# Kernel optimization log

Measured on AMD Instinct MI355X. Metric: run time of the kernel, lower is better.

Reference implementation:

```python
import jax, jax.numpy as jnp
import numpy as np

D_MODEL = 2048
NUM_HEADS = 32
NUM_GROUPS = 8
HEAD_DIM = D_MODEL // NUM_HEADS  # 64
HPG = NUM_HEADS // NUM_GROUPS    # heads per group = 4
B, S = 2, 2048


def setup_inputs() -> dict:
    key = jax.random.key(0)
    ks = jax.random.split(key, 11)
    sd = 1.0 / np.sqrt(D_MODEL)
    kv_dim = HEAD_DIM * NUM_GROUPS
    return {
        "q": jax.random.normal(ks[0], (B, S, D_MODEL), jnp.float32),
        "k": jax.random.normal(ks[1], (B, S, D_MODEL), jnp.float32),
        "v": jax.random.normal(ks[2], (B, S, D_MODEL), jnp.float32),
        "Wq": jax.random.normal(ks[3], (D_MODEL, D_MODEL), jnp.float32) * sd,
        "bq": jnp.zeros((D_MODEL,), jnp.float32),
        "Wk": jax.random.normal(ks[4], (D_MODEL, kv_dim), jnp.float32) * sd,
        "bk": jnp.zeros((kv_dim,), jnp.float32),
        "Wv": jax.random.normal(ks[5], (D_MODEL, kv_dim), jnp.float32) * sd,
        "bv": jnp.zeros((kv_dim,), jnp.float32),
        "Wo": jax.random.normal(ks[6], (D_MODEL, D_MODEL), jnp.float32) * sd,
        "bo": jnp.zeros((D_MODEL,), jnp.float32),
    }


def reference(q, k, v, Wq, bq, Wk, bk, Wv, bv, Wo, bo):
    b, qlen, _ = q.shape
    kvlen = k.shape[1]
    # projections
    qh = (q @ Wq + bq).reshape(b, qlen, NUM_GROUPS, HPG, HEAD_DIM)   # [b,s,g,h,d]
    kh = (k @ Wk + bk).reshape(b, kvlen, NUM_GROUPS, HEAD_DIM)        # [b,t,g,d]
    vh = (v @ Wv + bv).reshape(b, kvlen, NUM_GROUPS, HEAD_DIM)        # [b,t,g,d]
    scale = 1.0 / np.sqrt(HEAD_DIM).astype(np.float32)
    # grouped attention: each group's heads share the same K/V
    scores = jnp.einsum('bsghd,btgd->bghst', qh, kh) * scale          # [b,g,h,s,t]
    attn = jax.nn.softmax(scores, axis=-1)                            # dropout = identity (eval)
    out = jnp.einsum('bghst,btgd->bsghd', attn, vh)                   # [b,s,g,h,d]
    out = out.reshape(b, qlen, D_MODEL)
    return out @ Wo + bo
```

## Files before the change

### kernel.cpp

```cpp
#include <hip/hip_runtime.h>

typedef unsigned short u16;
typedef unsigned int u32;
typedef __attribute__((ext_vector_type(8))) short bf16x8;
typedef __attribute__((ext_vector_type(4))) float f32x4;
typedef __attribute__((ext_vector_type(16))) float f32x16;

#define DM 2048
#define SQ_SCALE (0.125f * 1.44269504089f)

__device__ __forceinline__ u16 f2bf(float f) {
  union { float f; u32 u; } v; v.f = f;
  u32 r = v.u + 0x7fffu + ((v.u >> 16) & 1u);
  return (u16)(r >> 16);
}
__device__ __forceinline__ u32 pkrn(float lo, float hi) {
  union { float f; u32 u; } a, b; a.f = lo; b.f = hi;
  return ((a.u + 0x8000u) >> 16) | ((b.u + 0x8000u) & 0xffff0000u);
}
__device__ __forceinline__ u32 cvtpk(float lo, float hi) {
  u32 r;
  asm("v_cvt_pk_bf16_f32 %0, %1, %2" : "=v"(r) : "v"(lo), "v"(hi));
  return r;
}
__device__ __forceinline__ void gload16(const u16* g, u16* l) {
  __builtin_amdgcn_global_load_lds((const __attribute__((address_space(1))) void*)g,
                                   (__attribute__((address_space(3))) void*)l, 16, 0, 0);
}

__global__ __launch_bounds__(256) void cast3(const float* __restrict__ a0,
                                             const float* __restrict__ a1,
                                             const float* __restrict__ a2,
                                             u16* __restrict__ o0,
                                             u16* __restrict__ o1,
                                             u16* __restrict__ o2) {
  const float* in; u16* out;
  if (blockIdx.z == 0) { in = a0; out = o0; }
  else if (blockIdx.z == 1) { in = a1; out = o1; }
  else { in = a2; out = o2; }
  size_t i = ((size_t)blockIdx.x * 256 + threadIdx.x) * 8;
  float4 f0 = *(const float4*)(in + i);
  float4 f1 = *(const float4*)(in + i + 4);
  uint4 w = {pkrn(f0.x, f0.y), pkrn(f0.z, f0.w), pkrn(f1.x, f1.y), pkrn(f1.z, f1.w)};
  *(uint4*)(out + i) = w;
}

__global__ __launch_bounds__(256) void transpose_cast(const float* __restrict__ in,
                                                      u16* __restrict__ out,
                                                      int K, int N) {
  __shared__ u16 s[64][72];
  int n0 = blockIdx.x * 64, k0 = blockIdx.y * 64;
  int t = threadIdx.x;
  int r = t >> 2;
  int cc = (t & 3) * 16;
  const float* ip = in + (size_t)(k0 + r) * N + n0 + cc;
  u16 tmp[16];
#pragma unroll
  for (int i = 0; i < 16; i += 4) {
    float4 v = *(const float4*)(ip + i);
    tmp[i] = f2bf(v.x); tmp[i + 1] = f2bf(v.y);
    tmp[i + 2] = f2bf(v.z); tmp[i + 3] = f2bf(v.w);
  }
  *(uint4*)&s[r][cc] = *(uint4*)tmp;
  *(uint4*)&s[r][cc + 8] = *(uint4*)(tmp + 8);
  __syncthreads();
#pragma unroll
  for (int i = 0; i < 16; i++) tmp[i] = s[cc + i][r];
  u16* op = out + (size_t)(n0 + r) * K + k0 + cc;
  *(uint4*)op = *(uint4*)tmp;
  *(uint4*)(op + 8) = *(uint4*)(tmp + 8);
}

__global__ __launch_bounds__(256) void gemm_proj(const u16* __restrict__ qb,
                                                 const u16* __restrict__ kb,
                                                 const u16* __restrict__ vb,
                                                 const u16* __restrict__ Bt,
                                                 const float* __restrict__ bqp,
                                                 const float* __restrict__ bkp,
                                                 const float* __restrict__ bvp,
                                                 u16* __restrict__ qhb,
                                                 u16* __restrict__ kvb,
                                                 u16* __restrict__ vtb) {
  __shared__ u16 As[128 * 32];
  __shared__ u16 Bs[128 * 32];
  int n0 = blockIdx.x * 128, m0 = blockIdx.y * 128;
  const u16* A; const float* bias; u16* C; int cw, bofs; float esc;
  if (n0 < 2048)      { A = qb; bias = bqp; C = qhb; cw = 2048; bofs = 0;    esc = SQ_SCALE; }
  else if (n0 < 2560) { A = kb; bias = bkp; C = kvb; cw = 1024; bofs = 2048; esc = 1.0f; }
  else                { A = vb; bias = bvp; C = kvb; cw = 1024; bofs = 2560; esc = 1.0f; }
  int ccol0 = (n0 < 2048) ? n0 : (n0 - 2048);

  int tid = threadIdx.x, wave = tid >> 6, lane = tid & 63;
  int lq = lane & 15, quad = lane >> 4;
  int wm = (wave & 1) * 64, wn = (wave >> 1) * 64;

  f32x4 zero = {0.f, 0.f, 0.f, 0.f};
  f32x4 acc[4][4];
#pragma unroll
  for (int i = 0; i < 4; i++)
#pragma unroll
    for (int j = 0; j < 4; j++) acc[i][j] = zero;

  const u16* gA = A + (size_t)(m0 + wave * 16 + (lane >> 2)) * 2048 + (lane & 3) * 8;
  const u16* gB = Bt + (size_t)(n0 + wave * 16 + (lane >> 2)) * 2048 + (lane & 3) * 8;
  u16* lA0 = &As[(wave * 16) * 32];
  u16* lA1 = &As[(64 + wave * 16) * 32];
  u16* lB0 = &Bs[(wave * 16) * 32];
  u16* lB1 = &Bs[(64 + wave * 16) * 32];

  for (int k0 = 0; k0 < 2048; k0 += 32) {
    __syncthreads();
    gload16(gA + k0, lA0);
    gload16(gA + (size_t)64 * 2048 + k0, lA1);
    gload16(gB + k0, lB0);
    gload16(gB + (size_t)64 * 2048 + k0, lB1);
    __syncthreads();
    bf16x8 af[4], bf[4];
#pragma unroll
    for (int i = 0; i < 4; i++) af[i] = *(const bf16x8*)&As[(wm + i * 16 + lq) * 32 + quad * 8];
#pragma unroll
    for (int j = 0; j < 4; j++) bf[j] = *(const bf16x8*)&Bs[(wn + j * 16 + lq) * 32 + quad * 8];
#pragma unroll
    for (int i = 0; i < 4; i++)
#pragma unroll
      for (int j = 0; j < 4; j++)
        acc[i][j] = __builtin_amdgcn_mfma_f32_16x16x32_bf16(af[i], bf[j], acc[i][j], 0, 0, 0);
  }
  if (n0 >= 2560) {
#pragma unroll
    for (int j = 0; j < 4; j++) {
      int cv = (n0 - 2560) + wn + j * 16 + lq;
      float bvv = bias[cv];
      u16* vout = vtb + (size_t)cv * 2048;
#pragma unroll
      for (int i = 0; i < 4; i++) {
        int row = m0 + wm + i * 16 + quad * 4;
        int bb = row >> 11, tt = row & 2047;
        u16 w4[4];
#pragma unroll
        for (int rg = 0; rg < 4; rg++) w4[rg] = f2bf(acc[i][j][rg] + bvv);
        *(uint2*)(vout + (size_t)bb * 8 * 64 * 2048 + tt) = *(uint2*)w4;
      }
    }
  } else {
#pragma unroll
    for (int j = 0; j < 4; j++) {
      int nglob = n0 + wn + j * 16 + lq;
      float bv = bias[nglob - bofs];
      int col = ccol0 + wn + j * 16 + lq;
#pragma unroll
      for (int i = 0; i < 4; i++) {
#pragma unroll
        for (int rg = 0; rg < 4; rg++) {
          int row = m0 + wm + i * 16 + quad * 4 + rg;
          C[(size_t)row * cw + col] = f2bf((acc[i][j][rg] + bv) * esc);
        }
      }
    }
  }
}

__global__ __launch_bounds__(256) void gemm_o(const u16* __restrict__ A,
                                              const u16* __restrict__ Bt,
                                              const float* __restrict__ bias,
                                              float* __restrict__ C) {
  __shared__ u16 As[128 * 32];
  __shared__ u16 Bs[128 * 32];
  int n0 = blockIdx.x * 128, m0 = blockIdx.y * 128;
  int tid = threadIdx.x, wave = tid >> 6, lane = tid & 63;
  int lq = lane & 15, quad = lane >> 4;
  int wm = (wave & 1) * 64, wn = (wave >> 1) * 64;

  f32x4 zero = {0.f, 0.f, 0.f, 0.f};
  f32x4 acc[4][4];
#pragma unroll
  for (int i = 0; i < 4; i++)
#pragma unroll
    for (int j = 0; j < 4; j++) acc[i][j] = zero;

  const u16* gA = A + (size_t)(m0 + wave * 16 + (lane >> 2)) * 2048 + (lane & 3) * 8;
  const u16* gB = Bt + (size_t)(n0 + wave * 16 + (lane >> 2)) * 2048 + (lane & 3) * 8;
  u16* lA0 = &As[(wave * 16) * 32];
  u16* lA1 = &As[(64 + wave * 16) * 32];
  u16* lB0 = &Bs[(wave * 16) * 32];
  u16* lB1 = &Bs[(64 + wave * 16) * 32];

  for (int k0 = 0; k0 < 2048; k0 += 32) {
    __syncthreads();
    gload16(gA + k0, lA0);
    gload16(gA + (size_t)64 * 2048 + k0, lA1);
    gload16(gB + k0, lB0);
    gload16(gB + (size_t)64 * 2048 + k0, lB1);
    __syncthreads();
    bf16x8 af[4], bf[4];
#pragma unroll
    for (int i = 0; i < 4; i++) af[i] = *(const bf16x8*)&As[(wm + i * 16 + lq) * 32 + quad * 8];
#pragma unroll
    for (int j = 0; j < 4; j++) bf[j] = *(const bf16x8*)&Bs[(wn + j * 16 + lq) * 32 + quad * 8];
#pragma unroll
    for (int i = 0; i < 4; i++)
#pragma unroll
      for (int j = 0; j < 4; j++)
        acc[i][j] = __builtin_amdgcn_mfma_f32_16x16x32_bf16(af[i], bf[j], acc[i][j], 0, 0, 0);
  }
#pragma unroll
  for (int j = 0; j < 4; j++) {
    int col = n0 + wn + j * 16 + lq;
    float bv = bias[col];
#pragma unroll
    for (int i = 0; i < 4; i++) {
#pragma unroll
      for (int rg = 0; rg < 4; rg++) {
        int row = m0 + wm + i * 16 + quad * 4 + rg;
        C[(size_t)row * 2048 + col] = acc[i][j][rg] + bv;
      }
    }
  }
}

__global__ __launch_bounds__(256) void attn2(const u16* __restrict__ qh,
                                             const u16* __restrict__ kvb,
                                             const u16* __restrict__ vtb,
                                             u16* __restrict__ out) {
  __shared__ u16 Ks[2][32][72];
  __shared__ u16 Vs[2][64][40];
  __shared__ float Ls[4][32];
  int flat = blockIdx.x + (blockIdx.y << 4);
  int w = ((flat & 7) << 7) + (flat >> 3);
  int head = w >> 4;
  int b = head >> 5, g = (head >> 2) & 7, h = head & 3;
  int tid = threadIdx.x, wave = tid >> 6, lane = tid & 63;
  int lh = lane & 31, hi = lane >> 5;
  const int qoff = (g * 4 + h) * 64;
  const int koff = g * 64;
  int sBase = (w & 15) * 128 + wave * 32;

  bf16x8 qf[4];
#pragma unroll
  for (int st = 0; st < 4; st++)
    qf[st] = *(const bf16x8*)(qh + (size_t)(b * 2048 + sBase + lh) * DM +
                              qoff + st * 16 + hi * 8);

  f32x16 o_acc[2];
#pragma unroll
  for (int db = 0; db < 2; db++)
#pragma unroll
    for (int r = 0; r < 16; r++) o_acc[db][r] = 0.f;
  float l_acc = 0.f;

  int sr = tid >> 3, sc = (tid & 7) * 8;
  int vd = tid >> 2, vc = (tid & 3) * 8;
  const u16* kbase = kvb + (size_t)b * 2048 * 1024 + koff;
  const u16* vbase = vtb + (size_t)(head >> 2) * 64 * 2048 + (size_t)vd * 2048;

  uint4 kreg = *(const uint4*)(kbase + (size_t)sr * 1024 + sc);
  uint4 vreg = *(const uint4*)(vbase + vc);

  int c = 0;
  for (int t0 = 0; t0 < 2048; t0 += 32) {
    *(uint4*)&Ks[c][sr][sc] = kreg;
    *(uint4*)&Vs[c][vd][vc] = vreg;
    int tn = (t0 + 32 < 2048) ? t0 + 32 : 0;
    kreg = *(const uint4*)(kbase + (size_t)(tn + sr) * 1024 + sc);
    vreg = *(const uint4*)(vbase + tn + vc);
    __syncthreads();

    bf16x8 kf[4], vf[2][2];
#pragma unroll
    for (int st = 0; st < 4; st++) kf[st] = *(const bf16x8*)&Ks[c][lh][st * 16 + hi * 8];
#pragma unroll
    for (int T = 0; T < 2; T++)
#pragma unroll
      for (int db = 0; db < 2; db++)
        vf[T][db] = *(const bf16x8*)&Vs[c][db * 32 + lh][T * 16 + hi * 8];

    f32x16 st_acc;
#pragma unroll
    for (int r = 0; r < 16; r++) st_acc[r] = 0.f;
    __builtin_amdgcn_s_setprio(1);
#pragma unroll
    for (int st = 0; st < 4; st++)
      st_acc = __builtin_amdgcn_mfma_f32_32x32x16_bf16(kf[st], qf[st], st_acc, 0, 0, 0);
    __builtin_amdgcn_s_setprio(0);
    float pr[16];
#pragma unroll
    for (int r = 0; r < 16; r++) pr[r] = __builtin_amdgcn_exp2f(st_acc[r]);
    float s0 = ((pr[0] + pr[1]) + (pr[2] + pr[3])) + ((pr[4] + pr[5]) + (pr[6] + pr[7]));
    float s1 = ((pr[8] + pr[9]) + (pr[10] + pr[11])) + ((pr[12] + pr[13]) + (pr[14] + pr[15]));
    l_acc += s0 + s1;
    u32 pk[8];
#pragma unroll
    for (int a = 0; a < 4; a++) {
      pk[2 * a] = cvtpk(pr[4 * a], pr[4 * a + 1]);
      pk[2 * a + 1] = cvtpk(pr[4 * a + 2], pr[4 * a + 3]);
    }
#pragma unroll
    for (int T = 0; T < 2; T++) {
      u32 E0 = hi ? pk[4 * T] : pk[4 * T + 2];
      u32 E1 = hi ? pk[4 * T + 1] : pk[4 * T + 3];
      u32 X0 = __shfl_xor(E0, 32);
      u32 X1 = __shfl_xor(E1, 32);
      union { u32 u[4]; bf16x8 v; } af;
      af.u[0] = hi ? X0 : pk[4 * T];
      af.u[1] = hi ? X1 : pk[4 * T + 1];
      af.u[2] = hi ? pk[4 * T + 2] : X0;
      af.u[3] = hi ? pk[4 * T + 3] : X1;
      __builtin_amdgcn_s_setprio(1);
#pragma unroll
      for (int db = 0; db < 2; db++)
        o_acc[db] = __builtin_amdgcn_mfma_f32_32x32x16_bf16(af.v, vf[T][db], o_acc[db], 0, 0, 0);
      __builtin_amdgcn_s_setprio(0);
    }
    c ^= 1;
  }

  {
    float lt = l_acc + __shfl_xor(l_acc, 32);
    Ls[wave][lh] = 1.0f / lt;
  }
  __builtin_amdgcn_wave_barrier();
  {
    f32x4 inv[4];
#pragma unroll
    for (int a = 0; a < 4; a++) inv[a] = *(const f32x4*)&Ls[wave][8 * a + 4 * hi];
#pragma unroll
    for (int db = 0; db < 2; db++) {
#pragma unroll
      for (int r = 0; r < 16; r++) {
        int srow = (r & 3) + 8 * (r >> 2) + 4 * hi;
        size_t o = (size_t)(b * 2048 + sBase + srow) * DM + qoff + db * 32 + lh;
        out[o] = f2bf(o_acc[db][r] * inv[r >> 2][r & 3]);
      }
    }
  }
}

extern "C" void kernel_launch(void* const* d_in, const int* in_sizes, int n_in,
                              void* d_out, int out_size, void* d_ws, size_t ws_size,
                              hipStream_t stream) {
  const float* q  = (const float*)d_in[0];
  const float* k  = (const float*)d_in[1];
  const float* v  = (const float*)d_in[2];
  const float* Wq = (const float*)d_in[3];
  const float* bq = (const float*)d_in[4];
  const float* Wk = (const float*)d_in[5];
  const float* bk = (const float*)d_in[6];
  const float* Wv = (const float*)d_in[7];
  const float* bv = (const float*)d_in[8];
  const float* Wo = (const float*)d_in[9];
  const float* bo = (const float*)d_in[10];

  u16* p = (u16*)d_ws;
  u16* WqkvT = p; p += (size_t)3072 * 2048;
  u16* WoT   = p; p += (size_t)2048 * 2048;
  u16* qb    = p; p += (size_t)4096 * 2048;
  u16* kb    = p; p += (size_t)4096 * 2048;
  u16* vb    = p; p += (size_t)4096 * 2048;
  u16* qhb   = p; p += (size_t)4096 * 2048;
  u16* kvb   = p; p += (size_t)4096 * 1024;
  u16* vtb   = p; p += (size_t)16 * 64 * 2048;
  u16* att   = qb;

  cast3<<<dim3(4096, 1, 3), 256, 0, stream>>>(q, k, v, qb, kb, vb);

  transpose_cast<<<dim3(32, 32), 256, 0, stream>>>(Wq, WqkvT, 2048, 2048);
  transpose_cast<<<dim3(8, 32), 256, 0, stream>>>(Wk, WqkvT + (size_t)2048 * 2048, 2048, 512);
  transpose_cast<<<dim3(8, 32), 256, 0, stream>>>(Wv, WqkvT + (size_t)2560 * 2048, 2048, 512);
  transpose_cast<<<dim3(32, 32), 256, 0, stream>>>(Wo, WoT, 2048, 2048);

  gemm_proj<<<dim3(24, 32), 256, 0, stream>>>(qb, kb, vb, WqkvT, bq, bk, bv, qhb, kvb, vtb);

  attn2<<<dim3(16, 64), 256, 0, stream>>>(qhb, kvb, vtb, att);

  gemm_o<<<dim3(16, 32), 256, 0, stream>>>(att, WoT, bo, (float*)d_out);
}
```

Before: 430.6 us.

## Fuse prep kernels into one launch, double K-step in GEMMs, reorder attn sync

Merges the input cast kernel and four weight transpose-cast kernels into a single prep launch, which removes four kernel launches and their tails. Both GEMM kernels now load two 32-wide K slices per iteration into doubled LDS buffers, halving the number of barrier pairs per tile at the cost of twice the LDS per block. The attention kernel moves its barrier ahead of the next-tile global prefetch. All three changes aim at launch and synchronisation overhead rather than arithmetic.

```diff
diff --git a/kernel.cpp b/kernel.cpp
--- a/kernel.cpp
+++ b/kernel.cpp
@@ -28,28 +28,38 @@
                                    (__attribute__((address_space(3))) void*)l, 16, 0, 0);
 }
 
-__global__ __launch_bounds__(256) void cast3(const float* __restrict__ a0,
-                                             const float* __restrict__ a1,
-                                             const float* __restrict__ a2,
-                                             u16* __restrict__ o0,
-                                             u16* __restrict__ o1,
-                                             u16* __restrict__ o2) {
-  const float* in; u16* out;
-  if (blockIdx.z == 0) { in = a0; out = o0; }
-  else if (blockIdx.z == 1) { in = a1; out = o1; }
-  else { in = a2; out = o2; }
-  size_t i = ((size_t)blockIdx.x * 256 + threadIdx.x) * 8;
-  float4 f0 = *(const float4*)(in + i);
-  float4 f1 = *(const float4*)(in + i + 4);
-  uint4 w = {pkrn(f0.x, f0.y), pkrn(f0.z, f0.w), pkrn(f1.x, f1.y), pkrn(f1.z, f1.w)};
-  *(uint4*)(out + i) = w;
-}
-
-__global__ __launch_bounds__(256) void transpose_cast(const float* __restrict__ in,
-                                                      u16* __restrict__ out,
-                                                      int K, int N) {
+__global__ __launch_bounds__(256) void prep(const float* __restrict__ q,
+                                            const float* __restrict__ k,
+                                            const float* __restrict__ v,
+                                            const float* __restrict__ Wq,
+                                            const float* __restrict__ Wk,
+                                            const float* __restrict__ Wv,
+                                            const float* __restrict__ Wo,
+                                            u16* __restrict__ qb,
+                                            u16* __restrict__ kb,
+                                            u16* __restrict__ vb,
+                                            u16* __restrict__ WqkvT,
+                                            u16* __restrict__ WoT) {
   __shared__ u16 s[64][72];
-  int n0 = blockIdx.x * 64, k0 = blockIdx.y * 64;
+  int bid = blockIdx.x;
+  if (bid < 12288) {
+    int z = bid >> 12, x = bid & 4095;
+    const float* in = (z == 0) ? q : (z == 1) ? k : v;
+    u16* out = (z == 0) ? qb : (z == 1) ? kb : vb;
+    size_t i = ((size_t)x * 256 + threadIdx.x) * 8;
+    float4 f0 = *(const float4*)(in + i);
+    float4 f1 = *(const float4*)(in + i + 4);
+    uint4 w = {pkrn(f0.x, f0.y), pkrn(f0.z, f0.w), pkrn(f1.x, f1.y), pkrn(f1.z, f1.w)};
+    *(uint4*)(out + i) = w;
+    return;
+  }
+  int off = bid - 12288;
+  const float* in; u16* out; int K, N, bx, by;
+  if (off < 1024)      { in = Wq; out = WqkvT;                          K = 2048; N = 2048; bx = off & 31; by = off >> 5; }
+  else if (off < 1280) { int i2 = off - 1024; in = Wk; out = WqkvT + (size_t)2048 * 2048; K = 2048; N = 512; bx = i2 & 7; by = i2 >> 3; }
+  else if (off < 1536) { int i2 = off - 1280; in = Wv; out = WqkvT + (size_t)2560 * 2048; K = 2048; N = 512; bx = i2 & 7; by = i2 >> 3; }
+  else                 { int i2 = off - 1536; in = Wo; out = WoT;       K = 2048; N = 2048; bx = i2 & 31; by = i2 >> 5; }
+  int n0 = bx * 64, k0 = by * 64;
   int t = threadIdx.x;
   int r = t >> 2;
   int cc = (t & 3) * 16;
@@ -57,9 +67,9 @@
   u16 tmp[16];
 #pragma unroll
   for (int i = 0; i < 16; i += 4) {
-    float4 v = *(const float4*)(ip + i);
-    tmp[i] = f2bf(v.x); tmp[i + 1] = f2bf(v.y);
-    tmp[i + 2] = f2bf(v.z); tmp[i + 3] = f2bf(v.w);
+    float4 vv = *(const float4*)(ip + i);
+    tmp[i] = f2bf(vv.x); tmp[i + 1] = f2bf(vv.y);
+    tmp[i + 2] = f2bf(vv.z); tmp[i + 3] = f2bf(vv.w);
   }
   *(uint4*)&s[r][cc] = *(uint4*)tmp;
   *(uint4*)&s[r][cc + 8] = *(uint4*)(tmp + 8);
@@ -81,8 +91,8 @@
                                                  u16* __restrict__ qhb,
                                                  u16* __restrict__ kvb,
                                                  u16* __restrict__ vtb) {
-  __shared__ u16 As[128 * 32];
-  __shared__ u16 Bs[128 * 32];
+  __shared__ u16 As[2][128 * 32];
+  __shared__ u16 Bs[2][128 * 32];
   int n0 = blockIdx.x * 128, m0 = blockIdx.y * 128;
   const u16* A; const float* bias; u16* C; int cw, bofs; float esc;
   if (n0 < 2048)      { A = qb; bias = bqp; C = qhb; cw = 2048; bofs = 0;    esc = SQ_SCALE; }
@@ -103,28 +113,35 @@
 
   const u16* gA = A + (size_t)(m0 + wave * 16 + (lane >> 2)) * 2048 + (lane & 3) * 8;
   const u16* gB = Bt + (size_t)(n0 + wave * 16 + (lane >> 2)) * 2048 + (lane & 3) * 8;
-  u16* lA0 = &As[(wave * 16) * 32];
-  u16* lA1 = &As[(64 + wave * 16) * 32];
-  u16* lB0 = &Bs[(wave * 16) * 32];
-  u16* lB1 = &Bs[(64 + wave * 16) * 32];
-
-  for (int k0 = 0; k0 < 2048; k0 += 32) {
-    __syncthreads();
-    gload16(gA + k0, lA0);
-    gload16(gA + (size_t)64 * 2048 + k0, lA1);
-    gload16(gB + k0, lB0);
-    gload16(gB + (size_t)64 * 2048 + k0, lB1);
-    __syncthreads();
-    bf16x8 af[4], bf[4];
-#pragma unroll
-    for (int i = 0; i < 4; i++) af[i] = *(const bf16x8*)&As[(wm + i * 16 + lq) * 32 + quad * 8];
-#pragma unroll
-    for (int j = 0; j < 4; j++) bf[j] = *(const bf16x8*)&Bs[(wn + j * 16 + lq) * 32 + quad * 8];
-#pragma unroll
-    for (int i = 0; i < 4; i++)
-#pragma unroll
-      for (int j = 0; j < 4; j++)
-        acc[i][j] = __builtin_amdgcn_mfma_f32_16x16x32_bf16(af[i], bf[j], acc[i][j], 0, 0, 0);
+  u16* lA0[2] = {&As[0][(wave * 16) * 32], &As[1][(wave * 16) * 32]};
+  u16* lA1[2] = {&As[0][(64 + wave * 16) * 32], &As[1][(64 + wave * 16) * 32]};
+  u16* lB0[2] = {&Bs[0][(wave * 16) * 32], &Bs[1][(wave * 16) * 32]};
+  u16* lB1[2] = {&Bs[0][(64 + wave * 16) * 32], &Bs[1][(64 + wave * 16) * 32]};
+
+  for (int k0 = 0; k0 < 2048; k0 += 64) {
+    __syncthreads();
+    gload16(gA + k0, lA0[0]);
+    gload16(gA + (size_t)64 * 2048 + k0, lA1[0]);
+    gload16(gA + k0 + 32, lA0[1]);
+    gload16(gA + (size_t)64 * 2048 + k0 + 32, lA1[1]);
+    gload16(gB + k0, lB0[0]);
+    gload16(gB + (size_t)64 * 2048 + k0, lB1[0]);
+    gload16(gB + k0 + 32, lB0[1]);
+    gload16(gB + (size_t)64 * 2048 + k0 + 32, lB1[1]);
+    __syncthreads();
+#pragma unroll
+    for (int hf = 0; hf < 2; hf++) {
+      bf16x8 af[4], bf[4];
+#pragma unroll
+      for (int i = 0; i < 4; i++) af[i] = *(const bf16x8*)&As[hf][(wm + i * 16 + lq) * 32 + quad * 8];
+#pragma unroll
+      for (int j = 0; j < 4; j++) bf[j] = *(const bf16x8*)&Bs[hf][(wn + j * 16 + lq) * 32 + quad * 8];
+#pragma unroll
+      for (int i = 0; i < 4; i++)
+#pragma unroll
+        for (int j = 0; j < 4; j++)
+          acc[i][j] = __builtin_amdgcn_mfma_f32_16x16x32_bf16(af[i], bf[j], acc[i][j], 0, 0, 0);
+    }
   }
   if (n0 >= 2560) {
 #pragma unroll
@@ -164,8 +181,8 @@
                                               const u16* __restrict__ Bt,
                                               const float* __restrict__ bias,
                                               float* __restrict__ C) {
-  __shared__ u16 As[128 * 32];
-  __shared__ u16 Bs[128 * 32];
+  __shared__ u16 As[2][128 * 32];
+  __shared__ u16 Bs[2][128 * 32];
   int n0 = blockIdx.x * 128, m0 = blockIdx.y * 128;
   int tid = threadIdx.x, wave = tid >> 6, lane = tid & 63;
   int lq = lane & 15, quad = lane >> 4;
@@ -180,28 +197,35 @@
 
   const u16* gA = A + (size_t)(m0 + wave * 16 + (lane >> 2)) * 2048 + (lane & 3) * 8;
   const u16* gB = Bt + (size_t)(n0 + wave * 16 + (lane >> 2)) * 2048 + (lane & 3) * 8;
-  u16* lA0 = &As[(wave * 16) * 32];
-  u16* lA1 = &As[(64 + wave * 16) * 32];
-  u16* lB0 = &Bs[(wave * 16) * 32];
-  u16* lB1 = &Bs[(64 + wave * 16) * 32];
-
-  for (int k0 = 0; k0 < 2048; k0 += 32) {
-    __syncthreads();
-    gload16(gA + k0, lA0);
-    gload16(gA + (size_t)64 * 2048 + k0, lA1);
-    gload16(gB + k0, lB0);
-    gload16(gB + (size_t)64 * 2048 + k0, lB1);
-    __syncthreads();
-    bf16x8 af[4], bf[4];
-#pragma unroll
-    for (int i = 0; i < 4; i++) af[i] = *(const bf16x8*)&As[(wm + i * 16 + lq) * 32 + quad * 8];
-#pragma unroll
-    for (int j = 0; j < 4; j++) bf[j] = *(const bf16x8*)&Bs[(wn + j * 16 + lq) * 32 + quad * 8];
-#pragma unroll
-    for (int i = 0; i < 4; i++)
-#pragma unroll
-      for (int j = 0; j < 4; j++)
-        acc[i][j] = __builtin_amdgcn_mfma_f32_16x16x32_bf16(af[i], bf[j], acc[i][j], 0, 0, 0);
+  u16* lA0[2] = {&As[0][(wave * 16) * 32], &As[1][(wave * 16) * 32]};
+  u16* lA1[2] = {&As[0][(64 + wave * 16) * 32], &As[1][(64 + wave * 16) * 32]};
+  u16* lB0[2] = {&Bs[0][(wave * 16) * 32], &Bs[1][(wave * 16) * 32]};
+  u16* lB1[2] = {&Bs[0][(64 + wave * 16) * 32], &Bs[1][(64 + wave * 16) * 32]};
+
+  for (int k0 = 0; k0 < 2048; k0 += 64) {
+    __syncthreads();
+    gload16(gA + k0, lA0[0]);
+    gload16(gA + (size_t)64 * 2048 + k0, lA1[0]);
+    gload16(gA + k0 + 32, lA0[1]);
+    gload16(gA + (size_t)64 * 2048 + k0 + 32, lA1[1]);
+    gload16(gB + k0, lB0[0]);
+    gload16(gB + (size_t)64 * 2048 + k0, lB1[0]);
+    gload16(gB + k0 + 32, lB0[1]);
+    gload16(gB + (size_t)64 * 2048 + k0 + 32, lB1[1]);
+    __syncthreads();
+#pragma unroll
+    for (int hf = 0; hf < 2; hf++) {
+      bf16x8 af[4], bf[4];
+#pragma unroll
+      for (int i = 0; i < 4; i++) af[i] = *(const bf16x8*)&As[hf][(wm + i * 16 + lq) * 32 + quad * 8];
+#pragma unroll
+      for (int j = 0; j < 4; j++) bf[j] = *(const bf16x8*)&Bs[hf][(wn + j * 16 + lq) * 32 + quad * 8];
+#pragma unroll
+      for (int i = 0; i < 4; i++)
+#pragma unroll
+        for (int j = 0; j < 4; j++)
+          acc[i][j] = __builtin_amdgcn_mfma_f32_16x16x32_bf16(af[i], bf[j], acc[i][j], 0, 0, 0);
+    }
   }
 #pragma unroll
   for (int j = 0; j < 4; j++) {
@@ -260,10 +284,10 @@
   for (int t0 = 0; t0 < 2048; t0 += 32) {
     *(uint4*)&Ks[c][sr][sc] = kreg;
     *(uint4*)&Vs[c][vd][vc] = vreg;
+    __syncthreads();
     int tn = (t0 + 32 < 2048) ? t0 + 32 : 0;
     kreg = *(const uint4*)(kbase + (size_t)(tn + sr) * 1024 + sc);
     vreg = *(const uint4*)(vbase + tn + vc);
-    __syncthreads();
 
     bf16x8 kf[4], vf[2][2];
 #pragma unroll
@@ -361,12 +385,7 @@
   u16* vtb   = p; p += (size_t)16 * 64 * 2048;
   u16* att   = qb;
 
-  cast3<<<dim3(4096, 1, 3), 256, 0, stream>>>(q, k, v, qb, kb, vb);
-
-  transpose_cast<<<dim3(32, 32), 256, 0, stream>>>(Wq, WqkvT, 2048, 2048);
-  transpose_cast<<<dim3(8, 32), 256, 0, stream>>>(Wk, WqkvT + (size_t)2048 * 2048, 2048, 512);
-  transpose_cast<<<dim3(8, 32), 256, 0, stream>>>(Wv, WqkvT + (size_t)2560 * 2048, 2048, 512);
-  transpose_cast<<<dim3(32, 32), 256, 0, stream>>>(Wo, WoT, 2048, 2048);
+  prep<<<dim3(14848), 256, 0, stream>>>(q, k, v, Wq, Wk, Wv, Wo, qb, kb, vb, WqkvT, WoT);
 
   gemm_proj<<<dim3(24, 32), 256, 0, stream>>>(qb, kb, vb, WqkvT, bq, bk, bv, qhb, kvb, vtb);
 
```

Measured after the change: 410.5 us. -4.7%, faster.
